# Kernel optimization log

Hardware: AMD Instinct MI355X
Metric: run time of the kernel (lower is better)

## Reference

```python
import jax, jax.numpy as jnp
import numpy as np

EPS = 1e-7
ROUTINGS = 3

def squash(s, axis=-1):
    # s: capsule vectors; squash along `axis`
    n2 = jnp.sum(s * s, axis=axis, keepdims=True)
    return (n2 / (1.0 + n2) / jnp.sqrt(n2 + EPS)) * s


def setup_inputs() -> dict:
    key = jax.random.key(0)
    k1, k2 = jax.random.split(key)
    B, N, O, Do, Di = 64, 1152, 32, 16, 8
    x = jax.random.normal(k1, (B, N, Di), dtype=jnp.float32)
    weight = 0.01 * jax.random.normal(k2, (N, O, Do, Di), dtype=jnp.float32)
    return {"x": x, "weight": weight}


def reference(x, weight):
    # x: [B, N, Di]; weight: [N, O, Do, Di]
    # x_hat[b,n,o,:] = weight[n,o] @ x[b,n]  -> [B, N, O, Do]
    x_hat = jnp.einsum('noij,bnj->bnoi', weight, x)
    x_hat_det = jax.lax.stop_gradient(x_hat)
    B, N, O, Do = x_hat.shape
    b = jnp.zeros((B, N, O), dtype=x_hat.dtype)
    vj = None
    for i in range(ROUTINGS):
        c = jax.nn.softmax(b, axis=2)  # [B, N, O] over output capsules
        xh = x_hat if i == ROUTINGS - 1 else x_hat_det
        s = jnp.einsum('bno,bnoi->boi', c, xh)  # sum over input capsules
        vj = squash(s, axis=-1)  # [B, O, Do]
        if i < ROUTINGS - 1:
            # agreement: <x_hat[b,n,o], vj[b,o]>
            b = b + jnp.einsum('bnoi,boi->bno', x_hat_det, vj)
    return vj  # [B, O, Do]
```

## Files before the change

kernel.cpp:

```cpp
#include <hip/hip_runtime.h>

#define Bb 64
#define Nn 1152
#define Oo 32
#define DOv 16
#define DIv 8
#define BPB 16

__device__ __forceinline__ void gload_lds16(const void* g, void* l) {
    __builtin_amdgcn_global_load_lds(
        (const __attribute__((address_space(1))) unsigned*)g,
        (__attribute__((address_space(3))) unsigned*)l, 16, 0, 0);
}

__global__ __launch_bounds__(256) void caps_route(
    const float* __restrict__ x,
    const float* __restrict__ w,
    const float* __restrict__ vcum,
    float* __restrict__ spart,
    int nc)
{
    const int t  = threadIdx.x;
    const int o  = t & 31;
    const int bl = t >> 5;
    const int n0 = blockIdx.x * nc;
    const int b0 = blockIdx.y * BPB;

    __shared__ float4 wbuf[2][1024];
    __shared__ float4 xbuf[16][BPB][2];

    int gq[4];
#pragma unroll
    for (int k = 0; k < 4; ++k) {
        int p = k * 256 + t;
        gq[k] = (p & ~31) | ((p ^ (p >> 5)) & 31);
    }

    auto stageW = [&](int n, int c) {
        const float4* wg = (const float4*)(w + (size_t)n * (Oo * DOv * DIv));
#pragma unroll
        for (int k = 0; k < 4; ++k)
            gload_lds16(&wg[gq[k]], &wbuf[c][k * 256 + t]);
    };
    auto stageX = [&](int nb) {
        int cnt = min(16, nc - nb);
        for (int q = t; q < cnt * 32; q += 256) {
            int nn = q >> 5, bb = (q >> 1) & 15, h = q & 1;
            xbuf[nn][bb][h] = ((const float4*)(
                x + ((size_t)(b0 + bb) * Nn + (size_t)(n0 + nb + nn)) * DIv))[h];
        }
    };

    const bool have_v = (vcum != nullptr);
    float vc0[DOv], vc1[DOv];
    if (have_v) {
#pragma unroll
        for (int i = 0; i < DOv; ++i) vc0[i] = vcum[((size_t)(b0 + bl) * Oo + o) * DOv + i];
#pragma unroll
        for (int i = 0; i < DOv; ++i) vc1[i] = vcum[((size_t)(b0 + 8 + bl) * Oo + o) * DOv + i];
    }

    float sacc0[DOv], sacc1[DOv];
#pragma unroll
    for (int i = 0; i < DOv; ++i) { sacc0[i] = 0.f; sacc1[i] = 0.f; }

    stageX(0);
    stageW(n0, 0);
    int cur = 0;

    for (int nn = 0; nn < nc; ++nn) {
        if (nn && (nn & 15) == 0) { __syncthreads(); stageX(nn); }
        __syncthreads();
        if (nn + 1 < nc) stageW(n0 + nn + 1, cur ^ 1);

        float4 xav0 = xbuf[nn & 15][bl][0],     xav1 = xbuf[nn & 15][bl][1];
        float4 xbv0 = xbuf[nn & 15][8 + bl][0], xbv1 = xbuf[nn & 15][8 + bl][1];
        float xa[8] = {xav0.x, xav0.y, xav0.z, xav0.w, xav1.x, xav1.y, xav1.z, xav1.w};
        float xb[8] = {xbv0.x, xbv0.y, xbv0.z, xbv0.w, xbv1.x, xbv1.y, xbv1.z, xbv1.w};

        float xh0[DOv], xh1[DOv];
#pragma unroll
        for (int i = 0; i < DOv; ++i) { xh0[i] = 0.f; xh1[i] = 0.f; }
#pragma unroll
        for (int i2 = 0; i2 < 32; ++i2) {
            float4 wv = wbuf[cur][o * 32 + (i2 ^ o)];
            const int i = i2 >> 1, jb = (i2 & 1) * 4;
            xh0[i] = fmaf(wv.x, xa[jb + 0], xh0[i]);
            xh0[i] = fmaf(wv.y, xa[jb + 1], xh0[i]);
            xh0[i] = fmaf(wv.z, xa[jb + 2], xh0[i]);
            xh0[i] = fmaf(wv.w, xa[jb + 3], xh0[i]);
            xh1[i] = fmaf(wv.x, xb[jb + 0], xh1[i]);
            xh1[i] = fmaf(wv.y, xb[jb + 1], xh1[i]);
            xh1[i] = fmaf(wv.z, xb[jb + 2], xh1[i]);
            xh1[i] = fmaf(wv.w, xb[jb + 3], xh1[i]);
        }

        float c0, c1;
        if (have_v) {
            float l0 = 0.f, l1 = 0.f;
#pragma unroll
            for (int i = 0; i < DOv; ++i) { l0 += xh0[i] * vc0[i]; l1 += xh1[i] * vc1[i]; }
            float m0 = l0, m1 = l1;
#pragma unroll
            for (int d = 16; d >= 1; d >>= 1) {
                m0 = fmaxf(m0, __shfl_xor(m0, d));
                m1 = fmaxf(m1, __shfl_xor(m1, d));
            }
            float e0 = __expf(l0 - m0), e1 = __expf(l1 - m1);
            float s0 = e0, s1 = e1;
#pragma unroll
            for (int d = 16; d >= 1; d >>= 1) {
                s0 += __shfl_xor(s0, d);
                s1 += __shfl_xor(s1, d);
            }
            c0 = e0 / s0; c1 = e1 / s1;
        } else {
            c0 = 1.0f / 32.0f; c1 = 1.0f / 32.0f;
        }

#pragma unroll
        for (int i = 0; i < DOv; ++i) { sacc0[i] += c0 * xh0[i]; sacc1[i] += c1 * xh1[i]; }
        cur ^= 1;
    }

    float* p  = spart + (size_t)blockIdx.x * (Bb * Oo * DOv);
    float* p0 = p + ((size_t)(b0 + bl) * Oo + o) * DOv;
    float* p1 = p + ((size_t)(b0 + 8 + bl) * Oo + o) * DOv;
#pragma unroll
    for (int i = 0; i < DOv; ++i) p0[i] = sacc0[i];
#pragma unroll
    for (int i = 0; i < DOv; ++i) p1[i] = sacc1[i];
}

__global__ __launch_bounds__(64) void caps_squash(
    const float* __restrict__ spart, int nch,
    const float* __restrict__ vin,
    float* __restrict__ vout,
    float* __restrict__ out)
{
    const int b = blockIdx.x, oo = blockIdx.y;
    const int t = threadIdx.x;
    const int i = t & 15, pg = t >> 4;
    const size_t base = ((size_t)b * Oo + oo) * DOv + i;
    float s = 0.f;
#pragma unroll 4
    for (int p = pg; p < nch; p += 4)
        s += spart[(size_t)p * (Bb * Oo * DOv) + base];
    s += __shfl_xor(s, 16);
    s += __shfl_xor(s, 32);
    float n2 = s * s;
#pragma unroll
    for (int d = 8; d >= 1; d >>= 1) n2 += __shfl_xor(n2, d);
    float vj = s * (n2 / ((1.f + n2) * sqrtf(n2 + 1e-7f)));
    if (t < 16) {
        if (vout) vout[base] = (vin ? vin[base] : 0.f) + vj;
        if (out)  out[base]  = vj;
    }
}

extern "C" void kernel_launch(void* const* d_in, const int* in_sizes, int n_in,
                              void* d_out, int out_size, void* d_ws, size_t ws_size,
                              hipStream_t stream)
{
    const float* x = (const float*)d_in[0];
    const float* w = (const float*)d_in[1];
    float* out = (float*)d_out;

    static const int cfgs[][2] = {{144,8},{72,16},{36,32},{18,64},{9,128},{4,288},{2,576},{1,1152}};
    int nch = 1, nc = 1152;
    for (auto& c : cfgs) {
        size_t need = ((size_t)c[0] * Bb * Oo * DOv + (size_t)Bb * Oo * DOv) * sizeof(float);
        if (need <= ws_size) { nch = c[0]; nc = c[1]; break; }
    }

    float* spart = (float*)d_ws;
    float* vcum  = spart + (size_t)nch * Bb * Oo * DOv;

    dim3 grid(nch, Bb / BPB), blk(256);
    dim3 sgrid(Bb, Oo), sblk(64);

    caps_route<<<grid, blk, 0, stream>>>(x, w, nullptr, spart, nc);
    caps_squash<<<sgrid, sblk, 0, stream>>>(spart, nch, nullptr, vcum, nullptr);
    caps_route<<<grid, blk, 0, stream>>>(x, w, vcum, spart, nc);
    caps_squash<<<sgrid, sblk, 0, stream>>>(spart, nch, vcum, vcum, nullptr);
    caps_route<<<grid, blk, 0, stream>>>(x, w, vcum, spart, nc);
    caps_squash<<<sgrid, sblk, 0, stream>>>(spart, nch, nullptr, nullptr, out);
}
```

Before: 104.5 us.

## Template routing kernel, triple-buffer weights, drop softmax max, vectorize squash

Makes the per-block input-capsule count a template parameter and fully unrolls the loop. Weight tiles are triple-buffered with explicit vmcnt waits and a raw barrier, and the block's x slice is preloaded once. The softmax max-reduction is removed, relying on small logits to avoid exp overflow. Partial-sum stores and the squash reduction kernel are vectorized with float4, and an occupancy hint of two blocks per CU is added. These changes cut synchronization, shuffles and memory instructions, at the cost of more LDS per block and reduced numerical safety in the softmax.

```diff
diff --git a/kernel.cpp b/kernel.cpp
--- a/kernel.cpp
+++ b/kernel.cpp
@@ -13,21 +13,21 @@
         (__attribute__((address_space(3))) unsigned*)l, 16, 0, 0);
 }
 
-__global__ __launch_bounds__(256) void caps_route(
+template<int NC>
+__global__ __launch_bounds__(256, 2) void caps_route(
     const float* __restrict__ x,
     const float* __restrict__ w,
     const float* __restrict__ vcum,
-    float* __restrict__ spart,
-    int nc)
+    float* __restrict__ spart)
 {
     const int t  = threadIdx.x;
     const int o  = t & 31;
     const int bl = t >> 5;
-    const int n0 = blockIdx.x * nc;
+    const int n0 = blockIdx.x * NC;
     const int b0 = blockIdx.y * BPB;
 
-    __shared__ float4 wbuf[2][1024];
-    __shared__ float4 xbuf[16][BPB][2];
+    __shared__ float4 wbuf[3][1024];
+    __shared__ float4 xbuf[NC][BPB][2];
 
     int gq[4];
 #pragma unroll
@@ -35,21 +35,18 @@
         int p = k * 256 + t;
         gq[k] = (p & ~31) | ((p ^ (p >> 5)) & 31);
     }
-
     auto stageW = [&](int n, int c) {
         const float4* wg = (const float4*)(w + (size_t)n * (Oo * DOv * DIv));
 #pragma unroll
         for (int k = 0; k < 4; ++k)
             gload_lds16(&wg[gq[k]], &wbuf[c][k * 256 + t]);
     };
-    auto stageX = [&](int nb) {
-        int cnt = min(16, nc - nb);
-        for (int q = t; q < cnt * 32; q += 256) {
-            int nn = q >> 5, bb = (q >> 1) & 15, h = q & 1;
-            xbuf[nn][bb][h] = ((const float4*)(
-                x + ((size_t)(b0 + bb) * Nn + (size_t)(n0 + nb + nn)) * DIv))[h];
-        }
-    };
+
+    for (int q = t; q < NC * BPB * 2; q += 256) {
+        int nn = q >> 5, bb = (q >> 1) & 15, h = q & 1;
+        xbuf[nn][bb][h] = ((const float4*)(
+            x + ((size_t)(b0 + bb) * Nn + (size_t)(n0 + nn)) * DIv))[h];
+    }
 
     const bool have_v = (vcum != nullptr);
     float vc0[DOv], vc1[DOv];
@@ -64,26 +61,28 @@
 #pragma unroll
     for (int i = 0; i < DOv; ++i) { sacc0[i] = 0.f; sacc1[i] = 0.f; }
 
-    stageX(0);
-    stageW(n0, 0);
-    int cur = 0;
-
-    for (int nn = 0; nn < nc; ++nn) {
-        if (nn && (nn & 15) == 0) { __syncthreads(); stageX(nn); }
-        __syncthreads();
-        if (nn + 1 < nc) stageW(n0 + nn + 1, cur ^ 1);
-
-        float4 xav0 = xbuf[nn & 15][bl][0],     xav1 = xbuf[nn & 15][bl][1];
-        float4 xbv0 = xbuf[nn & 15][8 + bl][0], xbv1 = xbuf[nn & 15][8 + bl][1];
-        float xa[8] = {xav0.x, xav0.y, xav0.z, xav0.w, xav1.x, xav1.y, xav1.z, xav1.w};
-        float xb[8] = {xbv0.x, xbv0.y, xbv0.z, xbv0.w, xbv1.x, xbv1.y, xbv1.z, xbv1.w};
+    __syncthreads();
+    stageW(n0 + 0, 0);
+    stageW(n0 + 1, 1);
+
+#pragma unroll
+    for (int nn = 0; nn < NC; ++nn) {
+        if (nn < NC - 1) asm volatile("s_waitcnt vmcnt(4)" ::: "memory");
+        else             asm volatile("s_waitcnt vmcnt(0)" ::: "memory");
+        __builtin_amdgcn_s_barrier();
+        if (nn + 2 < NC) stageW(n0 + nn + 2, (nn + 2) % 3);
+
+        const float* xs = (const float*)xbuf[nn];
+        float xa[DIv], xb[DIv];
+#pragma unroll
+        for (int j = 0; j < DIv; ++j) { xa[j] = xs[bl * DIv + j]; xb[j] = xs[(8 + bl) * DIv + j]; }
 
         float xh0[DOv], xh1[DOv];
 #pragma unroll
         for (int i = 0; i < DOv; ++i) { xh0[i] = 0.f; xh1[i] = 0.f; }
 #pragma unroll
         for (int i2 = 0; i2 < 32; ++i2) {
-            float4 wv = wbuf[cur][o * 32 + (i2 ^ o)];
+            float4 wv = wbuf[nn % 3][o * 32 + (i2 ^ o)];
             const int i = i2 >> 1, jb = (i2 & 1) * 4;
             xh0[i] = fmaf(wv.x, xa[jb + 0], xh0[i]);
             xh0[i] = fmaf(wv.y, xa[jb + 1], xh0[i]);
@@ -100,13 +99,7 @@
             float l0 = 0.f, l1 = 0.f;
 #pragma unroll
             for (int i = 0; i < DOv; ++i) { l0 += xh0[i] * vc0[i]; l1 += xh1[i] * vc1[i]; }
-            float m0 = l0, m1 = l1;
-#pragma unroll
-            for (int d = 16; d >= 1; d >>= 1) {
-                m0 = fmaxf(m0, __shfl_xor(m0, d));
-                m1 = fmaxf(m1, __shfl_xor(m1, d));
-            }
-            float e0 = __expf(l0 - m0), e1 = __expf(l1 - m1);
+            float e0 = __expf(l0), e1 = __expf(l1);
             float s0 = e0, s1 = e1;
 #pragma unroll
             for (int d = 16; d >= 1; d >>= 1) {
@@ -120,16 +113,17 @@
 
 #pragma unroll
         for (int i = 0; i < DOv; ++i) { sacc0[i] += c0 * xh0[i]; sacc1[i] += c1 * xh1[i]; }
-        cur ^= 1;
     }
 
     float* p  = spart + (size_t)blockIdx.x * (Bb * Oo * DOv);
     float* p0 = p + ((size_t)(b0 + bl) * Oo + o) * DOv;
     float* p1 = p + ((size_t)(b0 + 8 + bl) * Oo + o) * DOv;
 #pragma unroll
-    for (int i = 0; i < DOv; ++i) p0[i] = sacc0[i];
-#pragma unroll
-    for (int i = 0; i < DOv; ++i) p1[i] = sacc1[i];
+    for (int q = 0; q < 4; ++q)
+        ((float4*)p0)[q] = make_float4(sacc0[4*q], sacc0[4*q+1], sacc0[4*q+2], sacc0[4*q+3]);
+#pragma unroll
+    for (int q = 0; q < 4; ++q)
+        ((float4*)p1)[q] = make_float4(sacc1[4*q], sacc1[4*q+1], sacc1[4*q+2], sacc1[4*q+3]);
 }
 
 __global__ __launch_bounds__(64) void caps_squash(
@@ -140,21 +134,33 @@
 {
     const int b = blockIdx.x, oo = blockIdx.y;
     const int t = threadIdx.x;
-    const int i = t & 15, pg = t >> 4;
-    const size_t base = ((size_t)b * Oo + oo) * DOv + i;
-    float s = 0.f;
-#pragma unroll 4
-    for (int p = pg; p < nch; p += 4)
-        s += spart[(size_t)p * (Bb * Oo * DOv) + base];
-    s += __shfl_xor(s, 16);
-    s += __shfl_xor(s, 32);
-    float n2 = s * s;
-#pragma unroll
-    for (int d = 8; d >= 1; d >>= 1) n2 += __shfl_xor(n2, d);
-    float vj = s * (n2 / ((1.f + n2) * sqrtf(n2 + 1e-7f)));
-    if (t < 16) {
-        if (vout) vout[base] = (vin ? vin[base] : 0.f) + vj;
-        if (out)  out[base]  = vj;
+    const int q = t & 3, pg = t >> 2;
+    const size_t base4 = ((size_t)b * Oo + oo) * (DOv / 4) + q;
+    const float4* sp4 = (const float4*)spart;
+    const size_t chunk4 = (size_t)Bb * Oo * DOv / 4;
+
+    float4 s = make_float4(0.f, 0.f, 0.f, 0.f);
+    for (int p = pg; p < nch; p += 16) {
+        float4 v = sp4[(size_t)p * chunk4 + base4];
+        s.x += v.x; s.y += v.y; s.z += v.z; s.w += v.w;
+    }
+#pragma unroll
+    for (int d = 4; d <= 32; d <<= 1) {
+        s.x += __shfl_xor(s.x, d); s.y += __shfl_xor(s.y, d);
+        s.z += __shfl_xor(s.z, d); s.w += __shfl_xor(s.w, d);
+    }
+    float n2 = s.x * s.x + s.y * s.y + s.z * s.z + s.w * s.w;
+    n2 += __shfl_xor(n2, 1);
+    n2 += __shfl_xor(n2, 2);
+    float sc = n2 / ((1.f + n2) * sqrtf(n2 + 1e-7f));
+    if (t < 4) {
+        float4 vj = make_float4(s.x * sc, s.y * sc, s.z * sc, s.w * sc);
+        size_t i4 = base4;
+        if (vout) {
+            float4 vi = vin ? ((const float4*)vin)[i4] : make_float4(0.f, 0.f, 0.f, 0.f);
+            ((float4*)vout)[i4] = make_float4(vi.x + vj.x, vi.y + vj.y, vi.z + vj.z, vi.w + vj.w);
+        }
+        if (out) ((float4*)out)[i4] = vj;
     }
 }
 
@@ -166,23 +172,33 @@
     const float* w = (const float*)d_in[1];
     float* out = (float*)d_out;
 
-    static const int cfgs[][2] = {{144,8},{72,16},{36,32},{18,64},{9,128},{4,288},{2,576},{1,1152}};
-    int nch = 1, nc = 1152;
-    for (auto& c : cfgs) {
-        size_t need = ((size_t)c[0] * Bb * Oo * DOv + (size_t)Bb * Oo * DOv) * sizeof(float);
-        if (need <= ws_size) { nch = c[0]; nc = c[1]; break; }
+    int nch = 144;
+    size_t need = ((size_t)nch * Bb * Oo * DOv + (size_t)Bb * Oo * DOv) * sizeof(float);
+    if (need > ws_size) {
+        nch = 16;
     }
 
     float* spart = (float*)d_ws;
     float* vcum  = spart + (size_t)nch * Bb * Oo * DOv;
 
-    dim3 grid(nch, Bb / BPB), blk(256);
+    dim3 blk(256);
     dim3 sgrid(Bb, Oo), sblk(64);
 
-    caps_route<<<grid, blk, 0, stream>>>(x, w, nullptr, spart, nc);
-    caps_squash<<<sgrid, sblk, 0, stream>>>(spart, nch, nullptr, vcum, nullptr);
-    caps_route<<<grid, blk, 0, stream>>>(x, w, vcum, spart, nc);
-    caps_squash<<<sgrid, sblk, 0, stream>>>(spart, nch, vcum, vcum, nullptr);
-    caps_route<<<grid, blk, 0, stream>>>(x, w, vcum, spart, nc);
-    caps_squash<<<sgrid, sblk, 0, stream>>>(spart, nch, nullptr, nullptr, out);
-}
+    if (nch == 144) {
+        dim3 grid(144, Bb / BPB);
+        caps_route<8><<<grid, blk, 0, stream>>>(x, w, nullptr, spart);
+        caps_squash<<<sgrid, sblk, 0, stream>>>(spart, nch, nullptr, vcum, nullptr);
+        caps_route<8><<<grid, blk, 0, stream>>>(x, w, vcum, spart);
+        caps_squash<<<sgrid, sblk, 0, stream>>>(spart, nch, vcum, vcum, nullptr);
+        caps_route<8><<<grid, blk, 0, stream>>>(x, w, vcum, spart);
+        caps_squash<<<sgrid, sblk, 0, stream>>>(spart, nch, nullptr, nullptr, out);
+    } else {
+        dim3 grid(16, Bb / BPB);
+        caps_route<72><<<grid, blk, 0, stream>>>(x, w, nullptr, spart);
+        caps_squash<<<sgrid, sblk, 0, stream>>>(spart, nch, nullptr, vcum, nullptr);
+        caps_route<72><<<grid, blk, 0, stream>>>(x, w, vcum, spart);
+        caps_squash<<<sgrid, sblk, 0, stream>>>(spart, nch, vcum, vcum, nullptr);
+        caps_route<72><<<grid, blk, 0, stream>>>(x, w, vcum, spart);
+        caps_squash<<<sgrid, sblk, 0, stream>>>(spart, nch, nullptr, nullptr, out);
+    }
+}
```

Measured after the change: 196.6 us. 88.1% more time.
